# Kernel tuning notes

Hardware: AMD Instinct MI355X
Metric: run time of the kernel (lower is better)

## Reference

```python
import jax, jax.numpy as jnp
import numpy as np

T = 32  # simulation_length
L = 4   # number of NeuralCores in the chain


def to_uniform_spikes(x, cycle, sim_len):
    """Uniform spike encoding: emit round(x*T) spikes evenly spaced over T cycles.
    Faithful to SpikingUnifiedCoreFlow.to_uniform_spikes."""
    N = jnp.round(x * sim_len).astype(jnp.int32)
    mask = (N != 0) & (N != sim_len) & (cycle < sim_len)
    N_safe = jnp.maximum(N, 1)
    spacing = sim_len / N_safe.astype(x.dtype)          # T / N
    fire = mask & (jnp.floor(cycle / spacing) < N_safe) & (jnp.floor(jnp.mod(cycle, spacing)) == 0)
    out = fire.astype(x.dtype)
    return jnp.where(N == sim_len, jnp.ones_like(out), out)  # saturated channels fire every cycle


def setup_inputs() -> dict:
    key = jax.random.key(0)
    k0, k1 = jax.random.split(key)
    x = jax.random.uniform(k0, (128, 1024), dtype=jnp.float32)          # activations in [0,1]
    weights = jax.random.normal(k1, (L, 1024, 1024), dtype=jnp.float32) * 0.02  # (neurons, axons) per core
    thresholds = jnp.ones((L,), dtype=jnp.float32)
    return {"x": x, "weights": weights, "thresholds": thresholds}


def reference(x, weights, thresholds):
    """Rate-mode spiking simulation over a chain of NeuralCores.
    Per cycle: encode input to spikes (Uniform), propagate through cores with
    LIF integration (membrane += W @ spikes; spike = threshold < membrane;
    membrane -= spike * threshold), output = mean spike train of last core."""
    B = x.shape[0]
    H = weights.shape[1]

    def step(mem, cycle):
        sig = to_uniform_spikes(x, cycle, T)            # (B, axons_in)
        new_mems = []
        for l in range(L):
            m = mem[l] + sig @ weights[l].T             # F.linear(sig, W)
            s = (thresholds[l] < m).astype(x.dtype)     # thresholding_mode '<'
            m = m - s * thresholds[l]                   # Default firing: subtract reset
            new_mems.append(m)
            sig = s                                     # feed downstream core this cycle
        return jnp.stack(new_mems), sig                 # sig = last core spikes

    mem0 = jnp.zeros((L, B, H), dtype=x.dtype)
    _, out_spikes = jax.lax.scan(step, mem0, jnp.arange(T))  # (T, B, H)
    return out_spikes.mean(axis=0)                      # spike counts -> rates
```

## Files before the change

kernel.cpp:

```cpp
#include <hip/hip_runtime.h>
#include <stdint.h>


typedef __attribute__((ext_vector_type(4)))  int   i32x4;
typedef __attribute__((ext_vector_type(16))) int   i32x16;
typedef __attribute__((ext_vector_type(4)))  float f32x4;

#define SCALE_F 4294967296.0f
#define NSL 4

__device__ __forceinline__ void gload16(const void* g, void* l) {
    __builtin_amdgcn_global_load_lds(
        (const __attribute__((address_space(1))) void*)g,
        (__attribute__((address_space(3))) void*)l, 16, 0, 0);
}

__device__ __forceinline__ i32x4 expand16(unsigned int f) {
    i32x4 r;
    #pragma unroll
    for (int d = 0; d < 4; ++d)
        r[d] = (int)((((f >> (4 * d)) & 0xFu) * 0x00204081u) & 0x01010101u);
    return r;
}

__global__ void k_encode_t(const float* __restrict__ x, uint32_t* __restrict__ Am) {
    const int wid  = (blockIdx.x * 256 + threadIdx.x) >> 6;
    const int lane = threadIdx.x & 63;
    const int b = wid >> 4, kc = wid & 15;
    float v = x[b * 1024 + kc * 64 + lane];
    int N = (int)rintf(v * 32.0f);
    uint32_t bits = 0;
    if (N >= 32) {
        bits = 0xFFFFFFFFu;
    } else if (N > 0) {
        float spacing = 32.0f / (float)N;
        #pragma unroll
        for (int t = 0; t < 32; ++t) {
            float fm = fmodf((float)t, spacing);
            if (fm < 1.0f) bits |= (1u << t);
        }
    }
    uint32_t cap = 0;
    #pragma unroll
    for (int t = 0; t < 32; ++t) {
        unsigned long long bal = __ballot((bits >> t) & 1u);
        if (lane == t)      cap = (uint32_t)bal;
        if (lane == t + 32) cap = (uint32_t)(bal >> 32);
    }
    const int t = lane & 31, ww = lane >> 5;
    Am[(size_t)(b * 32 + t) * 32 + kc * 2 + ww] = cap;
}

__global__ void k_digits(const float* __restrict__ w, signed char* __restrict__ planes) {
    int tid = blockIdx.x * 256 + threadIdx.x;
    int l = tid >> 18;
    int rest4 = (tid & 0x3FFFF) << 2;
    f32x4 wv = *reinterpret_cast<const f32x4*>(w + ((size_t)l << 20) + rest4);
    long long q[4];
    #pragma unroll
    for (int i = 0; i < 4; ++i) q[i] = llrintf(wv[i] * SCALE_F);
    #pragma unroll
    for (int s = 0; s < NSL; ++s) {
        uint32_t pack = 0;
        #pragma unroll
        for (int i = 0; i < 4; ++i) {
            int d = (int)(signed char)((unsigned char)(q[i] & 255));
            q[i] = (q[i] - d) >> 8;
            pack |= ((uint32_t)(unsigned char)d) << (8 * i);
        }
        *reinterpret_cast<uint32_t*>(planes + (((size_t)(l * NSL + s)) << 20) + rest4) = pack;
    }
}

__global__ __launch_bounds__(512, 4) void k_fused(
        const uint32_t* __restrict__ Am,
        const signed char* __restrict__ planes,
        const float* __restrict__ th,
        uint32_t* __restrict__ AmNext,
        float* __restrict__ out,
        int layer) {
    __shared__ alignas(16) signed char lds[2][32768];

    const int tid  = threadIdx.x;
    const int lane = tid & 63;
    const int wave = tid >> 6;
    const int mw   = wave >> 1;
    const int nw   = wave & 1;
    const int lr   = lane & 31;
    const int hi   = lane >> 5;

    const int xc = blockIdx.x & 7, q = blockIdx.x >> 3;
    const int nTile = xc * 2 + (q & 1);
    const int mTile = q >> 1;
    const int mBase = mTile * 128, nBase = nTile * 64;

    const signed char* srcB[NSL];
    {
        const int r0 = tid >> 3, qs = tid & 7;
        const int sw0 = (qs ^ (r0 & 7)) * 16;
        #pragma unroll
        for (int s = 0; s < NSL; ++s)
            srcB[s] = planes + (((size_t)(layer * NSL + s)) << 20)
                    + (size_t)(nBase + r0) * 1024 + sw0;
    }
    const uint32_t* aRow = Am + (size_t)(mBase + mw * 32 + lr) * 32;

    int baddr[4];
    {
        const int brow = nw * 32 + lr;
        #pragma unroll
        for (int ks = 0; ks < 4; ++ks)
            baddr[ks] = brow * 128 + (((ks * 2 + hi) ^ (brow & 7)) * 16);
    }

    i32x16 acc[NSL];
    #pragma unroll
    for (int s = 0; s < NSL; ++s)
        #pragma unroll
        for (int r = 0; r < 16; ++r) acc[s][r] = 0;

    auto H0 = [&](int buf, int c) {
        const int ko = c * 128;
        gload16(srcB[0] + ko, &lds[buf][0]    + tid * 16);
        gload16(srcB[1] + ko, &lds[buf][8192] + tid * 16);
    };
    auto H1 = [&](int buf, int c) {
        const int ko = c * 128;
        gload16(srcB[2] + ko, &lds[buf][16384] + tid * 16);
        gload16(srcB[3] + ko, &lds[buf][24576] + tid * 16);
    };

    i32x4 amr[2];
    amr[0] = *reinterpret_cast<const i32x4*>(aRow);
    H0(0, 0);
    H1(0, 0);

    #pragma unroll
    for (int c = 0; c < 8; ++c) {
        const int buf = c & 1;
        const signed char* lb = &lds[buf][0];

        asm volatile("s_waitcnt vmcnt(2)" ::: "memory");
        __builtin_amdgcn_s_barrier();
        asm volatile("" ::: "memory");

        if (c + 1 < 8) {
            H0(buf ^ 1, c + 1);
            amr[(c + 1) & 1] = *reinterpret_cast<const i32x4*>(aRow + (c + 1) * 4);
        }

        i32x4 af[4];
        __builtin_amdgcn_s_setprio(1);
        #pragma unroll
        for (int ks = 0; ks < 4; ++ks) {
            af[ks] = expand16((((unsigned)amr[c & 1][ks]) >> (16 * hi)) & 0xFFFFu);
            #pragma unroll
            for (int s = 0; s < 2; ++s) {
                i32x4 bf = *reinterpret_cast<const i32x4*>(lb + s * 8192 + baddr[ks]);
                acc[s] = __builtin_amdgcn_mfma_i32_32x32x32_i8(af[ks], bf, acc[s], 0, 0, 0);
            }
        }
        __builtin_amdgcn_s_setprio(0);

        if (c + 1 < 8) asm volatile("s_waitcnt vmcnt(3)" ::: "memory");
        else           asm volatile("s_waitcnt vmcnt(0)" ::: "memory");
        __builtin_amdgcn_s_barrier();
        asm volatile("" ::: "memory");

        if (c + 1 < 8) H1(buf ^ 1, c + 1);

        __builtin_amdgcn_s_setprio(1);
        #pragma unroll
        for (int ks = 0; ks < 4; ++ks) {
            #pragma unroll
            for (int s = 0; s < 2; ++s) {
                i32x4 bf = *reinterpret_cast<const i32x4*>(lb + (2 + s) * 8192 + baddr[ks]);
                acc[2 + s] = __builtin_amdgcn_mfma_i32_32x32x32_i8(af[ks], bf, acc[2 + s], 0, 0, 0);
            }
        }
        __builtin_amdgcn_s_setprio(0);
    }

    const long long TH = llrintf(th[layer] * SCALE_F);
    const int batch = mTile * 4 + mw;
    uint32_t bits = 0;
    long long mmem = 0;
    #pragma unroll
    for (int half = 0; half < 2; ++half) {
        long long own[8], par[8];
        #pragma unroll
        for (int r = 0; r < 8; ++r) {
            long long v = 0;
            #pragma unroll
            for (int s = 0; s < NSL; ++s)
                v += ((long long)acc[s][half * 8 + r]) << (8 * s);
            own[r] = v;
        }
        #pragma unroll
        for (int r = 0; r < 8; ++r) {
            int plo = __shfl((int)(uint32_t)own[r], lane ^ 32, 64);
            int phi = __shfl((int)(own[r] >> 32), lane ^ 32, 64);
            par[r] = ((long long)phi << 32) | (uint32_t)plo;
        }
        #pragma unroll
        for (int tq = 0; tq < 16; ++tq) {
            const int idx = (tq >> 3) * 4 + (tq & 3);
            const int usePar = ((tq >> 2) & 1) ^ hi;
            long long v = usePar ? par[idx] : own[idx];
            mmem += v;
            if (mmem > TH) { mmem -= TH; bits |= (1u << (half * 16 + tq)); }
        }
    }

    if (AmNext) {
        uint32_t cap = 0;
        #pragma unroll
        for (int t = 0; t < 32; ++t) {
            unsigned long long bal = __ballot((bits >> t) & 1u);
            if (lane == t) cap = (uint32_t)bal;
        }
        if (hi == 0)
            AmNext[(size_t)(batch * 32 + lr) * 32 + nTile * 2 + nw] = cap;
    } else if (hi == 0) {
        out[batch * 1024 + nBase + nw * 32 + lr] = (float)__popc(bits) * 0.03125f;
    }
}

extern "C" void kernel_launch(void* const* d_in, const int* in_sizes, int n_in,
                              void* d_out, int out_size, void* d_ws, size_t ws_size,
                              hipStream_t stream) {
    const float* x  = (const float*)d_in[0];
    const float* w  = (const float*)d_in[1];
    const float* th = (const float*)d_in[2];
    float* out = (float*)d_out;
    char* ws = (char*)d_ws;

    signed char* planes = (signed char*)(ws);
    uint32_t*    Am0    = (uint32_t*)(ws + 16777216);
    uint32_t*    Am1    = (uint32_t*)(ws + 17301504);

    k_encode_t<<<512, 256, 0, stream>>>(x, Am0);
    k_digits<<<4096, 256, 0, stream>>>(w, planes);

    uint32_t* Ain = Am0;
    uint32_t* Anx = Am1;
    for (int l = 0; l < 4; ++l) {
        k_fused<<<512, 512, 0, stream>>>(Ain, planes, th,
                                         (l < 3) ? Anx : nullptr,
                                         (l == 3) ? out : nullptr, l);
        uint32_t* tmp = Ain; Ain = Anx; Anx = tmp;
    }
}
```

Baseline: 106.4 us.

## Split digit planes across wave groups, reuse B fragments over two M rows

Merges the encode and digit-split kernels into one launch. In the fused GEMM, each wave group now handles two of the four weight digit planes and two 32-row M sub-tiles, so every B fragment read from LDS feeds two MFMAs. Partial sums are combined through an LDS exchange before the LIF threshold scan. The whole stage is now loaded at once with a single barrier per chunk plus a trailing barrier. This adds an LDS round trip and extra syncs, and raises accumulator register pressure.

```diff
diff --git a/kernel.cpp b/kernel.cpp
--- a/kernel.cpp
+++ b/kernel.cpp
@@ -23,52 +23,53 @@
     return r;
 }
 
-__global__ void k_encode_t(const float* __restrict__ x, uint32_t* __restrict__ Am) {
-    const int wid  = (blockIdx.x * 256 + threadIdx.x) >> 6;
-    const int lane = threadIdx.x & 63;
-    const int b = wid >> 4, kc = wid & 15;
-    float v = x[b * 1024 + kc * 64 + lane];
-    int N = (int)rintf(v * 32.0f);
-    uint32_t bits = 0;
-    if (N >= 32) {
-        bits = 0xFFFFFFFFu;
-    } else if (N > 0) {
-        float spacing = 32.0f / (float)N;
+__global__ void k_prep(const float* __restrict__ x, const float* __restrict__ w,
+                       uint32_t* __restrict__ Am, signed char* __restrict__ planes) {
+    if (blockIdx.x < 4096) {
+        int tid = blockIdx.x * 256 + threadIdx.x;
+        int l = tid >> 18;
+        int rest4 = (tid & 0x3FFFF) << 2;
+        f32x4 wv = *reinterpret_cast<const f32x4*>(w + ((size_t)l << 20) + rest4);
+        long long q[4];
+        #pragma unroll
+        for (int i = 0; i < 4; ++i) q[i] = llrintf(wv[i] * SCALE_F);
+        #pragma unroll
+        for (int s = 0; s < NSL; ++s) {
+            uint32_t pack = 0;
+            #pragma unroll
+            for (int i = 0; i < 4; ++i) {
+                int d = (int)(signed char)((unsigned char)(q[i] & 255));
+                q[i] = (q[i] - d) >> 8;
+                pack |= ((uint32_t)(unsigned char)d) << (8 * i);
+            }
+            *reinterpret_cast<uint32_t*>(planes + (((size_t)(l * NSL + s)) << 20) + rest4) = pack;
+        }
+    } else {
+        const int wid  = ((blockIdx.x - 4096) * 256 + threadIdx.x) >> 6;
+        const int lane = threadIdx.x & 63;
+        const int b = wid >> 4, kc = wid & 15;
+        float v = x[b * 1024 + kc * 64 + lane];
+        int N = (int)rintf(v * 32.0f);
+        uint32_t bits = 0;
+        if (N >= 32) {
+            bits = 0xFFFFFFFFu;
+        } else if (N > 0) {
+            float spacing = 32.0f / (float)N;
+            #pragma unroll
+            for (int t = 0; t < 32; ++t) {
+                float fm = fmodf((float)t, spacing);
+                if (fm < 1.0f) bits |= (1u << t);
+            }
+        }
+        uint32_t cap = 0;
         #pragma unroll
         for (int t = 0; t < 32; ++t) {
-            float fm = fmodf((float)t, spacing);
-            if (fm < 1.0f) bits |= (1u << t);
-        }
-    }
-    uint32_t cap = 0;
-    #pragma unroll
-    for (int t = 0; t < 32; ++t) {
-        unsigned long long bal = __ballot((bits >> t) & 1u);
-        if (lane == t)      cap = (uint32_t)bal;
-        if (lane == t + 32) cap = (uint32_t)(bal >> 32);
-    }
-    const int t = lane & 31, ww = lane >> 5;
-    Am[(size_t)(b * 32 + t) * 32 + kc * 2 + ww] = cap;
-}
-
-__global__ void k_digits(const float* __restrict__ w, signed char* __restrict__ planes) {
-    int tid = blockIdx.x * 256 + threadIdx.x;
-    int l = tid >> 18;
-    int rest4 = (tid & 0x3FFFF) << 2;
-    f32x4 wv = *reinterpret_cast<const f32x4*>(w + ((size_t)l << 20) + rest4);
-    long long q[4];
-    #pragma unroll
-    for (int i = 0; i < 4; ++i) q[i] = llrintf(wv[i] * SCALE_F);
-    #pragma unroll
-    for (int s = 0; s < NSL; ++s) {
-        uint32_t pack = 0;
-        #pragma unroll
-        for (int i = 0; i < 4; ++i) {
-            int d = (int)(signed char)((unsigned char)(q[i] & 255));
-            q[i] = (q[i] - d) >> 8;
-            pack |= ((uint32_t)(unsigned char)d) << (8 * i);
-        }
-        *reinterpret_cast<uint32_t*>(planes + (((size_t)(l * NSL + s)) << 20) + rest4) = pack;
+            unsigned long long bal = __ballot((bits >> t) & 1u);
+            if (lane == t)      cap = (uint32_t)bal;
+            if (lane == t + 32) cap = (uint32_t)(bal >> 32);
+        }
+        const int t = lane & 31, ww = lane >> 5;
+        Am[(size_t)(b * 32 + t) * 32 + kc * 2 + ww] = cap;
     }
 }
 
@@ -84,7 +85,8 @@
     const int tid  = threadIdx.x;
     const int lane = tid & 63;
     const int wave = tid >> 6;
-    const int mw   = wave >> 1;
+    const int sg   = wave >> 2;
+    const int mw   = (wave >> 1) & 1;
     const int nw   = wave & 1;
     const int lr   = lane & 31;
     const int hi   = lane >> 5;
@@ -103,7 +105,8 @@
             srcB[s] = planes + (((size_t)(layer * NSL + s)) << 20)
                     + (size_t)(nBase + r0) * 1024 + sw0;
     }
-    const uint32_t* aRow = Am + (size_t)(mBase + mw * 32 + lr) * 32;
+    const uint32_t* aRow0 = Am + (size_t)(mBase + mw * 64 + lr) * 32;
+    const uint32_t* aRow1 = aRow0 + 32 * 32;
 
     int baddr[4];
     {
@@ -113,100 +116,115 @@
             baddr[ks] = brow * 128 + (((ks * 2 + hi) ^ (brow & 7)) * 16);
     }
 
-    i32x16 acc[NSL];
-    #pragma unroll
-    for (int s = 0; s < NSL; ++s)
-        #pragma unroll
-        for (int r = 0; r < 16; ++r) acc[s][r] = 0;
-
-    auto H0 = [&](int buf, int c) {
+    i32x16 acc[2][2];
+    #pragma unroll
+    for (int m = 0; m < 2; ++m)
+        #pragma unroll
+        for (int s = 0; s < 2; ++s)
+            #pragma unroll
+            for (int r = 0; r < 16; ++r) acc[m][s][r] = 0;
+
+    auto STAGE = [&](int buf, int c) {
         const int ko = c * 128;
-        gload16(srcB[0] + ko, &lds[buf][0]    + tid * 16);
-        gload16(srcB[1] + ko, &lds[buf][8192] + tid * 16);
-    };
-    auto H1 = [&](int buf, int c) {
-        const int ko = c * 128;
+        gload16(srcB[0] + ko, &lds[buf][0]     + tid * 16);
+        gload16(srcB[1] + ko, &lds[buf][8192]  + tid * 16);
         gload16(srcB[2] + ko, &lds[buf][16384] + tid * 16);
         gload16(srcB[3] + ko, &lds[buf][24576] + tid * 16);
     };
 
-    i32x4 amr[2];
-    amr[0] = *reinterpret_cast<const i32x4*>(aRow);
-    H0(0, 0);
-    H1(0, 0);
+    i32x4 amr0[2], amr1[2];
+    STAGE(0, 0);
+    amr0[0] = *reinterpret_cast<const i32x4*>(aRow0);
+    amr1[0] = *reinterpret_cast<const i32x4*>(aRow1);
 
     #pragma unroll
     for (int c = 0; c < 8; ++c) {
         const int buf = c & 1;
         const signed char* lb = &lds[buf][0];
 
-        asm volatile("s_waitcnt vmcnt(2)" ::: "memory");
-        __builtin_amdgcn_s_barrier();
-        asm volatile("" ::: "memory");
-
         if (c + 1 < 8) {
-            H0(buf ^ 1, c + 1);
-            amr[(c + 1) & 1] = *reinterpret_cast<const i32x4*>(aRow + (c + 1) * 4);
-        }
-
-        i32x4 af[4];
-        __builtin_amdgcn_s_setprio(1);
-        #pragma unroll
-        for (int ks = 0; ks < 4; ++ks) {
-            af[ks] = expand16((((unsigned)amr[c & 1][ks]) >> (16 * hi)) & 0xFFFFu);
-            #pragma unroll
-            for (int s = 0; s < 2; ++s) {
-                i32x4 bf = *reinterpret_cast<const i32x4*>(lb + s * 8192 + baddr[ks]);
-                acc[s] = __builtin_amdgcn_mfma_i32_32x32x32_i8(af[ks], bf, acc[s], 0, 0, 0);
-            }
-        }
-        __builtin_amdgcn_s_setprio(0);
-
-        if (c + 1 < 8) asm volatile("s_waitcnt vmcnt(3)" ::: "memory");
+            STAGE(buf ^ 1, c + 1);
+            amr0[(c + 1) & 1] = *reinterpret_cast<const i32x4*>(aRow0 + (c + 1) * 4);
+            amr1[(c + 1) & 1] = *reinterpret_cast<const i32x4*>(aRow1 + (c + 1) * 4);
+        }
+
+        if (c + 1 < 8) asm volatile("s_waitcnt vmcnt(6)" ::: "memory");
         else           asm volatile("s_waitcnt vmcnt(0)" ::: "memory");
         __builtin_amdgcn_s_barrier();
         asm volatile("" ::: "memory");
 
-        if (c + 1 < 8) H1(buf ^ 1, c + 1);
-
         __builtin_amdgcn_s_setprio(1);
         #pragma unroll
         for (int ks = 0; ks < 4; ++ks) {
+            i32x4 af0 = expand16((((unsigned)amr0[c & 1][ks]) >> (16 * hi)) & 0xFFFFu);
+            i32x4 af1 = expand16((((unsigned)amr1[c & 1][ks]) >> (16 * hi)) & 0xFFFFu);
             #pragma unroll
             for (int s = 0; s < 2; ++s) {
-                i32x4 bf = *reinterpret_cast<const i32x4*>(lb + (2 + s) * 8192 + baddr[ks]);
-                acc[2 + s] = __builtin_amdgcn_mfma_i32_32x32x32_i8(af[ks], bf, acc[2 + s], 0, 0, 0);
+                i32x4 bf = *reinterpret_cast<const i32x4*>(
+                        lb + (sg * 2 + s) * 8192 + baddr[ks]);
+                acc[0][s] = __builtin_amdgcn_mfma_i32_32x32x32_i8(af0, bf, acc[0][s], 0, 0, 0);
+                acc[1][s] = __builtin_amdgcn_mfma_i32_32x32x32_i8(af1, bf, acc[1][s], 0, 0, 0);
             }
         }
         __builtin_amdgcn_s_setprio(0);
+
+        __builtin_amdgcn_s_barrier();
+        asm volatile("" ::: "memory");
+    }
+
+    long long pKeep[16], pSend[16];
+    #pragma unroll
+    for (int r = 0; r < 16; ++r) {
+        long long v0 = (long long)acc[0][0][r] + ((long long)acc[0][1][r] << 8);
+        long long v1 = (long long)acc[1][0][r] + ((long long)acc[1][1][r] << 8);
+        pKeep[r] = sg ? v1 : v0;
+        pSend[r] = sg ? v0 : v1;
+    }
+
+    signed char* ex = &lds[0][0];
+    const int pr = (mw * 2 + nw);
+    const int reg_w = (pr * 2 + sg) * 8192;
+    const int reg_r = (pr * 2 + (sg ^ 1)) * 8192;
+    #pragma unroll
+    for (int u = 0; u < 8; ++u) {
+        i32x4 wv;
+        long long a = pSend[2 * u], b = pSend[2 * u + 1];
+        wv[0] = (int)a; wv[1] = (int)(a >> 32);
+        wv[2] = (int)b; wv[3] = (int)(b >> 32);
+        *reinterpret_cast<i32x4*>(ex + reg_w + lane * 128 + ((u ^ (lane & 7)) * 16)) = wv;
+    }
+    __syncthreads();
+    long long tot[16];
+    #pragma unroll
+    for (int u = 0; u < 8; ++u) {
+        i32x4 v = *reinterpret_cast<const i32x4*>(
+                ex + reg_r + lane * 128 + ((u ^ (lane & 7)) * 16));
+        long long a = ((long long)v[1] << 32) | (uint32_t)v[0];
+        long long b = ((long long)v[3] << 32) | (uint32_t)v[2];
+        tot[2 * u]     = sg ? (pKeep[2 * u]     << 16) + a : pKeep[2 * u]     + (a << 16);
+        tot[2 * u + 1] = sg ? (pKeep[2 * u + 1] << 16) + b : pKeep[2 * u + 1] + (b << 16);
     }
 
     const long long TH = llrintf(th[layer] * SCALE_F);
-    const int batch = mTile * 4 + mw;
+    const int batch = mTile * 4 + mw * 2 + sg;
     uint32_t bits = 0;
     long long mmem = 0;
     #pragma unroll
     for (int half = 0; half < 2; ++half) {
-        long long own[8], par[8];
+        long long own_[8], par[8];
+        #pragma unroll
+        for (int r = 0; r < 8; ++r) own_[r] = tot[half * 8 + r];
         #pragma unroll
         for (int r = 0; r < 8; ++r) {
-            long long v = 0;
-            #pragma unroll
-            for (int s = 0; s < NSL; ++s)
-                v += ((long long)acc[s][half * 8 + r]) << (8 * s);
-            own[r] = v;
-        }
-        #pragma unroll
-        for (int r = 0; r < 8; ++r) {
-            int plo = __shfl((int)(uint32_t)own[r], lane ^ 32, 64);
-            int phi = __shfl((int)(own[r] >> 32), lane ^ 32, 64);
+            int plo = __shfl((int)(uint32_t)own_[r], lane ^ 32, 64);
+            int phi = __shfl((int)(own_[r] >> 32), lane ^ 32, 64);
             par[r] = ((long long)phi << 32) | (uint32_t)plo;
         }
         #pragma unroll
         for (int tq = 0; tq < 16; ++tq) {
             const int idx = (tq >> 3) * 4 + (tq & 3);
             const int usePar = ((tq >> 2) & 1) ^ hi;
-            long long v = usePar ? par[idx] : own[idx];
+            long long v = usePar ? par[idx] : own_[idx];
             mmem += v;
             if (mmem > TH) { mmem -= TH; bits |= (1u << (half * 16 + tq)); }
         }
@@ -239,8 +257,7 @@
     uint32_t*    Am0    = (uint32_t*)(ws + 16777216);
     uint32_t*    Am1    = (uint32_t*)(ws + 17301504);
 
-    k_encode_t<<<512, 256, 0, stream>>>(x, Am0);
-    k_digits<<<4096, 256, 0, stream>>>(w, planes);
+    k_prep<<<4608, 256, 0, stream>>>(x, w, Am0, planes);
 
     uint32_t* Ain = Am0;
     uint32_t* Anx = Am1;
```

Measured after the change: 114.5 us. +7.6%, slower.
